# Kernel optimization log

Measured on AMD Instinct MI355X. Metric: run time of the kernel, lower is better.

The kernel has to match this reference:

```python
import jax, jax.numpy as jnp
import numpy as np

B, T, C = 2, 192, 512
H, D = 8, 64  # num_heads, head_dim; inner_dim = H*D = C


def setup_inputs() -> dict:
    key = jax.random.key(0)
    k1, k2, k3 = jax.random.split(key, 3)
    x = jax.random.normal(k1, (B, T, C), dtype=jnp.float32)
    W_in = jax.random.normal(k2, (C, 5 * H * D), dtype=jnp.float32) * 0.02
    b_in = jnp.zeros((5 * H * D,), dtype=jnp.float32)
    W_out = jax.random.normal(k3, (H * D, C), dtype=jnp.float32) * 0.02
    b_out = jnp.zeros((C,), dtype=jnp.float32)
    return {"x": x, "W_in": W_in, "b_in": b_in, "W_out": W_out, "b_out": b_out}


def _split_heads(t):
    # (B,T,H*D) -> (B,H,T,D)
    return t.reshape(B, T, H, D).transpose(0, 2, 1, 3)


def reference(x, W_in, b_in, W_out, b_out):
    scale = D ** -0.5
    proj = x @ W_in + b_in  # (B,T,5*H*D)
    q, k1, v1, k2, v2 = jnp.split(proj, 5, axis=-1)
    q = _split_heads(q) * scale
    k1 = _split_heads(k1)
    v1 = _split_heads(v1)
    k2 = _split_heads(k2)
    v2 = _split_heads(v2)
    # trilinear logits: <q_i, k1_j, k2_k> / sqrt(D), computed in fp32
    logits = jnp.einsum('bhid,bhjd,bhkd->bhijk', q, k1, k2,
                        preferred_element_type=jnp.float32)
    # softmax over the joint (j,k) axes
    attn = jax.nn.softmax(logits.reshape(B, H, T, T * T), axis=-1)
    attn = attn.reshape(B, H, T, T, T).astype(x.dtype)
    # out_i[d] = sum_{j,k} attn[i,j,k] * v1_j[d] * v2_k[d]
    out = jnp.einsum('bhijk,bhjd,bhkd->bhid', attn, v1, v2)
    y = out.transpose(0, 2, 1, 3).reshape(B, T, H * D)  # merge heads
    return y @ W_out + b_out
```

## Files before the change

kernel.cpp:

```cpp
#include <hip/hip_runtime.h>


typedef float  v4f __attribute__((ext_vector_type(4)));
typedef short  v8s __attribute__((ext_vector_type(8)));

__device__ __forceinline__ unsigned short f2bf(float f) {
  unsigned u = __float_as_uint(f);
  u += 0x7fffu + ((u >> 16) & 1u);
  return (unsigned short)(u >> 16);
}
__device__ __forceinline__ float bf2f(unsigned short b) {
  return __uint_as_float(((unsigned)b) << 16);
}

#if __has_builtin(__builtin_amdgcn_exp2f)
#define EXP2F(x) __builtin_amdgcn_exp2f(x)
#else
#define EXP2F(x) exp2f(x)
#endif

#define MFMA32(a, b, c) __builtin_amdgcn_mfma_f32_16x16x32_bf16((a), (b), (c), 0, 0, 0)

#define QSCALE 0.18033688011112042f


#define XH_OFF   589824
#define XL_OFF   786432
#define WTH_OFF  983040
#define WTL_OFF  2293760
#define WOTH_OFF 3604480
#define WOTL_OFF 3866624
#define OH_OFF   4128768
#define OL_OFF   4325376

__global__ __launch_bounds__(256) void prep_kernel(
    const float* __restrict__ x, const float* __restrict__ Win,
    const float* __restrict__ Wout, unsigned short* __restrict__ wsh) {
  const int bi = blockIdx.x, t = threadIdx.x;
  if (bi < 768) {
    const float* W; unsigned short *Th, *Tl; int R, n0, k0;
    if (bi < 640) {
      W = Win; Th = wsh + WTH_OFF; Tl = wsh + WTL_OFF; R = 2560;
      n0 = (bi % 40) << 6; k0 = (bi / 40) << 5;
    } else {
      const int idx = bi - 640;
      W = Wout; Th = wsh + WOTH_OFF; Tl = wsh + WOTL_OFF; R = 512;
      n0 = (idx & 7) << 6; k0 = (idx >> 3) << 5;
    }
    const int n = n0 + (t & 63);
    const int kg = k0 + (t >> 6) * 8;
    float v[8];
#pragma unroll
    for (int j = 0; j < 8; ++j) v[j] = W[(kg + j) * R + n];
    union { uint4 u; unsigned short us[8]; } ph, pl;
#pragma unroll
    for (int j = 0; j < 8; ++j) {
      const unsigned short h = f2bf(v[j]);
      ph.us[j] = h;
      pl.us[j] = f2bf(v[j] - bf2f(h));
    }
    *(uint4*)(Th + n * 512 + kg) = ph.u;
    *(uint4*)(Tl + n * 512 + kg) = pl.u;
  } else {
    const int flat = ((bi - 768) * 256 + t) * 8;
    const v4f v0 = *(const v4f*)(x + flat);
    const v4f v1 = *(const v4f*)(x + flat + 4);
    union { uint4 u; unsigned short us[8]; } ph, pl;
#pragma unroll
    for (int j = 0; j < 4; ++j) {
      unsigned short h = f2bf(v0[j]);
      ph.us[j] = h; pl.us[j] = f2bf(v0[j] - bf2f(h));
      h = f2bf(v1[j]);
      ph.us[4 + j] = h; pl.us[4 + j] = f2bf(v1[j] - bf2f(h));
    }
    *(uint4*)(wsh + XH_OFF + flat) = ph.u;
    *(uint4*)(wsh + XL_OFF + flat) = pl.u;
  }
}

__global__ __launch_bounds__(64) void proj_kernel(
    const unsigned short* __restrict__ wsh, const float* __restrict__ bin,
    float* __restrict__ wsf, unsigned short* __restrict__ wshd) {
  const int lane = threadIdx.x;
  const int c = lane & 15, q = lane >> 4;
  const int bm = blockIdx.x % 12, bn = blockIdx.x / 12;

  const unsigned short* ah0 = wsh + XH_OFF + (bm * 32 + c) * 512 + (q << 3);
  const unsigned short* ah1 = ah0 + 16 * 512;
  const unsigned short* al0 = wsh + XL_OFF + (bm * 32 + c) * 512 + (q << 3);
  const unsigned short* al1 = al0 + 16 * 512;
  const unsigned short* bh0 = wsh + WTH_OFF + (bn * 32 + c) * 512 + (q << 3);
  const unsigned short* bh1 = bh0 + 16 * 512;
  const unsigned short* bl0 = wsh + WTL_OFF + (bn * 32 + c) * 512 + (q << 3);
  const unsigned short* bl1 = bl0 + 16 * 512;

  const v4f z = {0.f, 0.f, 0.f, 0.f};
  v4f a00 = z, a01 = z, a10 = z, a11 = z;

  v8s cAh0 = *(const v8s*)ah0, cAh1 = *(const v8s*)ah1;
  v8s cAl0 = *(const v8s*)al0, cAl1 = *(const v8s*)al1;
  v8s cBh0 = *(const v8s*)bh0, cBh1 = *(const v8s*)bh1;
  v8s cBl0 = *(const v8s*)bl0, cBl1 = *(const v8s*)bl1;

#pragma unroll 1
  for (int ks = 0; ks < 16; ++ks) {
    v8s nAh0, nAh1, nAl0, nAl1, nBh0, nBh1, nBl0, nBl1;
    if (ks < 15) {
      const int o = (ks + 1) * 32;
      nAh0 = *(const v8s*)(ah0 + o); nAh1 = *(const v8s*)(ah1 + o);
      nAl0 = *(const v8s*)(al0 + o); nAl1 = *(const v8s*)(al1 + o);
      nBh0 = *(const v8s*)(bh0 + o); nBh1 = *(const v8s*)(bh1 + o);
      nBl0 = *(const v8s*)(bl0 + o); nBl1 = *(const v8s*)(bl1 + o);
    }
    a00 = MFMA32(cAl0, cBh0, a00); a00 = MFMA32(cAh0, cBl0, a00); a00 = MFMA32(cAh0, cBh0, a00);
    a01 = MFMA32(cAl0, cBh1, a01); a01 = MFMA32(cAh0, cBl1, a01); a01 = MFMA32(cAh0, cBh1, a01);
    a10 = MFMA32(cAl1, cBh0, a10); a10 = MFMA32(cAh1, cBl0, a10); a10 = MFMA32(cAh1, cBh0, a10);
    a11 = MFMA32(cAl1, cBh1, a11); a11 = MFMA32(cAh1, cBl1, a11); a11 = MFMA32(cAh1, cBh1, a11);
    cAh0 = nAh0; cAh1 = nAh1; cAl0 = nAl0; cAl1 = nAl1;
    cBh0 = nBh0; cBh1 = nBh1; cBl0 = nBl0; cBl1 = nBl1;
  }

  v4f accs[2][2] = {{a00, a01}, {a10, a11}};
#pragma unroll
  for (int mt = 0; mt < 2; ++mt) {
#pragma unroll
    for (int nt = 0; nt < 2; ++nt) {
      const int n = bn * 32 + nt * 16 + c;
      const int which = n >> 9, cc = n & 511, h = cc >> 6, d = cc & 63;
      const float bv = bin[n];
#pragma unroll
      for (int r = 0; r < 4; ++r) {
        const int m = bm * 32 + mt * 16 + (q << 2) + r;
        const int b = (m >= 192) ? 1 : 0;
        const int tt = m - (b ? 192 : 0);
        const int bh = b * 8 + h;
        const float val = accs[mt][nt][r] + bv;
        const int rm = ((bh * 192 + tt) << 6) + d;
        if (which == 0)      wsf[rm] = val * QSCALE;
        else if (which == 1) wshd[rm] = f2bf(val);
        else if (which == 2) wshd[393216 + ((bh << 6) + d) * 192 + tt] = f2bf(val);
        else if (which == 3) wshd[196608 + rm] = f2bf(val);
        else wsf[196608 + ((bh * 192 + tt) * 16 + (d & 15)) * 4 + (d >> 4)] = val;
      }
    }
  }
}

__global__ __launch_bounds__(256, 2) void attn_kernel(
    const float* __restrict__ wsf, const unsigned short* __restrict__ wsh,
    float* __restrict__ accp, float* __restrict__ Sp) {
  __shared__ unsigned short smem[64 * 200 + 4 * 16 * 40];
  unsigned short* V1s = smem;

  const int tid  = threadIdx.x;
  const int wv   = tid >> 6;
  const int lane = tid & 63;
  const int c    = lane & 15;
  const int quad = lane >> 4;

  const int bb = blockIdx.x;
  const int kb = bb & 3;
  const int it = (bb >> 2) % 12;
  const int bh = bb / 48;

  const unsigned short* k1g = wsh + bh * 192 * 64;
  const unsigned short* v1g = wsh + 393216 + bh * 64 * 192;
  const unsigned short* k2g = wsh + 196608 + bh * 192 * 64;
  const float*          v2g = wsf + 196608 + bh * 12288;

  for (int idx = tid; idx < 1536; idx += 256) {
    const int r = idx / 24, c8 = (idx % 24) * 8;
    *(uint4*)(V1s + r * 200 + c8) = *(const uint4*)(v1g + r * 192 + c8);
  }

  v8s k1f[12][2];
#pragma unroll
  for (int jt = 0; jt < 12; ++jt) {
    const unsigned short* kp = k1g + ((jt * 16 + c) << 6) + (quad << 3);
    k1f[jt][0] = *(const v8s*)(kp);
    k1f[jt][1] = *(const v8s*)(kp + 32);
  }

  const float* qg = wsf + ((bh * 192 + it * 16 + c) << 6) + (quad << 3);
  float q0[8], q1[8];
  {
    v4f qa = *(const v4f*)(qg), qb = *(const v4f*)(qg + 4);
    v4f qc = *(const v4f*)(qg + 32), qd = *(const v4f*)(qg + 36);
#pragma unroll
    for (int e = 0; e < 4; ++e) {
      q0[e] = qa[e]; q0[4 + e] = qb[e];
      q1[e] = qc[e]; q1[4 + e] = qd[e];
    }
  }
  __syncthreads();

  unsigned short* Pch = smem + 12800 + wv * 640;
  const v4f z = {0.f, 0.f, 0.f, 0.f};
  v4f acc0 = z, acc1 = z, acc2 = z, acc3 = z;
  float S0 = 0.f, S1 = 0.f, S2 = 0.f, S3 = 0.f;

  const int kstart = kb * 48 + wv * 12;
  union { uint4 u4; unsigned short us[8]; } kl, kh, nkl, nkh;
  kl.u4 = *(const uint4*)(k2g + (kstart << 6) + (quad << 3));
  kh.u4 = *(const uint4*)(k2g + (kstart << 6) + (quad << 3) + 32);
  v4f v2 = *(const v4f*)(v2g + ((kstart * 16 + c) << 2));

  for (int s = 0; s < 12; ++s) {
    v4f nv2;
    if (s < 11) {
      const int k2o = ((kstart + s + 1) << 6) + (quad << 3);
      nkl.u4 = *(const uint4*)(k2g + k2o);
      nkh.u4 = *(const uint4*)(k2g + k2o + 32);
      nv2 = *(const v4f*)(v2g + (((kstart + s + 1) * 16 + c) << 2));
    }

    union { v8s v; unsigned short us[8]; } af0, af1;
#pragma unroll
    for (int e = 0; e < 8; ++e) {
      af0.us[e] = f2bf(q0[e] * bf2f(kl.us[e]));
      af1.us[e] = f2bf(q1[e] * bf2f(kh.us[e]));
    }

    v4f o0 = z, o1 = z, o2 = z, o3 = z;
#pragma unroll
    for (int jp = 0; jp < 6; ++jp) {
#pragma unroll
      for (int jj2 = 0; jj2 < 2; ++jj2) {
        const int jt = jp * 2 + jj2;
        v4f Cf = MFMA32(af0.v, k1f[jt][0], z);
        Cf = MFMA32(af1.v, k1f[jt][1], Cf);
        unsigned short* wp2 = Pch + (quad << 2) * 40 + jj2 * 16 + c;
        const float p0 = EXP2F(Cf[0]), p1 = EXP2F(Cf[1]);
        const float p2 = EXP2F(Cf[2]), p3 = EXP2F(Cf[3]);
        S0 += p0; S1 += p1; S2 += p2; S3 += p3;
        wp2[0]   = (unsigned short)(__float_as_uint(p0) >> 16);
        wp2[40]  = (unsigned short)(__float_as_uint(p1) >> 16);
        wp2[80]  = (unsigned short)(__float_as_uint(p2) >> 16);
        wp2[120] = (unsigned short)(__float_as_uint(p3) >> 16);
      }
      const v8s ap = *(const v8s*)(Pch + c * 40 + (quad << 3));
      const int vcol = jp * 32 + (quad << 3);
      o0 = MFMA32(ap, *(const v8s*)(V1s + (c)      * 200 + vcol), o0);
      o1 = MFMA32(ap, *(const v8s*)(V1s + (c + 16) * 200 + vcol), o1);
      o2 = MFMA32(ap, *(const v8s*)(V1s + (c + 32) * 200 + vcol), o2);
      o3 = MFMA32(ap, *(const v8s*)(V1s + (c + 48) * 200 + vcol), o3);
    }
    acc0 += o0 * v2[0]; acc1 += o1 * v2[1]; acc2 += o2 * v2[2]; acc3 += o3 * v2[3];
    kl = nkl; kh = nkh; v2 = nv2;
  }

  __syncthreads();
  float* redA = (float*)smem;
  float* redS = (float*)smem + 4096;

#pragma unroll
  for (int m2 = 1; m2 < 16; m2 <<= 1) {
    S0 += __shfl_xor(S0, m2, 16);
    S1 += __shfl_xor(S1, m2, 16);
    S2 += __shfl_xor(S2, m2, 16);
    S3 += __shfl_xor(S3, m2, 16);
  }
  if (c == 0) {
    float* rs = redS + wv * 16 + (quad << 2);
    rs[0] = S0; rs[1] = S1; rs[2] = S2; rs[3] = S3;
  }
#pragma unroll
  for (int r = 0; r < 4; ++r) {
    float* rr = redA + wv * 1024 + (((quad << 2) + r) << 6) + c;
    rr[0] = acc0[r]; rr[16] = acc1[r]; rr[32] = acc2[r]; rr[48] = acc3[r];
  }
  __syncthreads();

  const int pbase = (bh * 12 + it) * 4 + kb;
  float* ap_out = accp + pbase * 1024;
  for (int idx = tid; idx < 1024; idx += 256)
    ap_out[idx] = redA[idx] + redA[1024 + idx] + redA[2048 + idx] + redA[3072 + idx];
  if (tid < 16)
    Sp[pbase * 16 + tid] = redS[tid] + redS[16 + tid] + redS[32 + tid] + redS[48 + tid];
}

__global__ __launch_bounds__(256) void norm_kernel(
    const float* __restrict__ accp, const float* __restrict__ Sp,
    unsigned short* __restrict__ wsh) {
  const int flat = blockIdx.x * 2048 + threadIdx.x * 8;
  const int m = flat >> 9, cc = flat & 511;
  const int b = (m >= 192) ? 1 : 0;
  const int tt = m - (b ? 192 : 0);
  const int h = cc >> 6, d0 = cc & 63;
  const int bh = b * 8 + h, it = tt >> 4, i = tt & 15;
  const int pb = (bh * 12 + it) * 4;
  const float* ap = accp + pb * 1024 + (i << 6) + d0;
  v4f a0 = *(const v4f*)(ap), a1 = *(const v4f*)(ap + 4);
  float Sv = Sp[pb * 16 + i];
#pragma unroll
  for (int kb = 1; kb < 4; ++kb) {
    a0 += *(const v4f*)(ap + kb * 1024);
    a1 += *(const v4f*)(ap + kb * 1024 + 4);
    Sv += Sp[(pb + kb) * 16 + i];
  }
  const float inv = 1.0f / Sv;
  union { uint4 u; unsigned short us[8]; } ph, pl;
#pragma unroll
  for (int j = 0; j < 4; ++j) {
    float v = a0[j] * inv;
    unsigned short hh = f2bf(v);
    ph.us[j] = hh; pl.us[j] = f2bf(v - bf2f(hh));
    v = a1[j] * inv;
    hh = f2bf(v);
    ph.us[4 + j] = hh; pl.us[4 + j] = f2bf(v - bf2f(hh));
  }
  *(uint4*)(wsh + OH_OFF + flat) = ph.u;
  *(uint4*)(wsh + OL_OFF + flat) = pl.u;
}

__global__ __launch_bounds__(64) void outp_kernel(
    const unsigned short* __restrict__ wsh, const float* __restrict__ bout,
    float* __restrict__ y) {
  const int lane = threadIdx.x;
  const int c = lane & 15, q = lane >> 4;
  const int bm = blockIdx.x % 12, bn = blockIdx.x / 12;

  const unsigned short* ah0 = wsh + OH_OFF + (bm * 32 + c) * 512 + (q << 3);
  const unsigned short* ah1 = ah0 + 16 * 512;
  const unsigned short* al0 = wsh + OL_OFF + (bm * 32 + c) * 512 + (q << 3);
  const unsigned short* al1 = al0 + 16 * 512;
  const unsigned short* bh0 = wsh + WOTH_OFF + (bn * 32 + c) * 512 + (q << 3);
  const unsigned short* bh1 = bh0 + 16 * 512;
  const unsigned short* bl0 = wsh + WOTL_OFF + (bn * 32 + c) * 512 + (q << 3);
  const unsigned short* bl1 = bl0 + 16 * 512;

  const v4f z = {0.f, 0.f, 0.f, 0.f};
  v4f a00 = z, a01 = z, a10 = z, a11 = z;

  v8s cAh0 = *(const v8s*)ah0, cAh1 = *(const v8s*)ah1;
  v8s cAl0 = *(const v8s*)al0, cAl1 = *(const v8s*)al1;
  v8s cBh0 = *(const v8s*)bh0, cBh1 = *(const v8s*)bh1;
  v8s cBl0 = *(const v8s*)bl0, cBl1 = *(const v8s*)bl1;

#pragma unroll 1
  for (int ks = 0; ks < 16; ++ks) {
    v8s nAh0, nAh1, nAl0, nAl1, nBh0, nBh1, nBl0, nBl1;
    if (ks < 15) {
      const int o = (ks + 1) * 32;
      nAh0 = *(const v8s*)(ah0 + o); nAh1 = *(const v8s*)(ah1 + o);
      nAl0 = *(const v8s*)(al0 + o); nAl1 = *(const v8s*)(al1 + o);
      nBh0 = *(const v8s*)(bh0 + o); nBh1 = *(const v8s*)(bh1 + o);
      nBl0 = *(const v8s*)(bl0 + o); nBl1 = *(const v8s*)(bl1 + o);
    }
    a00 = MFMA32(cAl0, cBh0, a00); a00 = MFMA32(cAh0, cBl0, a00); a00 = MFMA32(cAh0, cBh0, a00);
    a01 = MFMA32(cAl0, cBh1, a01); a01 = MFMA32(cAh0, cBl1, a01); a01 = MFMA32(cAh0, cBh1, a01);
    a10 = MFMA32(cAl1, cBh0, a10); a10 = MFMA32(cAh1, cBl0, a10); a10 = MFMA32(cAh1, cBh0, a10);
    a11 = MFMA32(cAl1, cBh1, a11); a11 = MFMA32(cAh1, cBl1, a11); a11 = MFMA32(cAh1, cBh1, a11);
    cAh0 = nAh0; cAh1 = nAh1; cAl0 = nAl0; cAl1 = nAl1;
    cBh0 = nBh0; cBh1 = nBh1; cBl0 = nBl0; cBl1 = nBl1;
  }

  v4f accs[2][2] = {{a00, a01}, {a10, a11}};
#pragma unroll
  for (int mt = 0; mt < 2; ++mt) {
#pragma unroll
    for (int nt = 0; nt < 2; ++nt) {
      const int n = bn * 32 + nt * 16 + c;
      const float bv = bout[n];
#pragma unroll
      for (int r = 0; r < 4; ++r) {
        const int m = bm * 32 + mt * 16 + (q << 2) + r;
        y[m * 512 + n] = accs[mt][nt][r] + bv;
      }
    }
  }
}

extern "C" void kernel_launch(void* const* d_in, const int* in_sizes, int n_in,
                              void* d_out, int out_size, void* d_ws, size_t ws_size,
                              hipStream_t stream) {
  const float* x    = (const float*)d_in[0];
  const float* Win  = (const float*)d_in[1];
  const float* bin  = (const float*)d_in[2];
  const float* Wout = (const float*)d_in[3];
  const float* bout = (const float*)d_in[4];

  float* wsf = (float*)d_ws;
  unsigned short* wsh = (unsigned short*)(wsf + 1191936);
  float* accp = wsf + 393216;
  float* Sp   = wsf + 1179648;

  prep_kernel<<<dim3(864), 256, 0, stream>>>(x, Win, Wout, wsh);
  proj_kernel<<<dim3(960), 64, 0, stream>>>(wsh, bin, wsf, wsh);
  attn_kernel<<<dim3(768), 256, 0, stream>>>(wsf, wsh, accp, Sp);
  norm_kernel<<<dim3(96), 256, 0, stream>>>(accp, Sp, wsh);
  outp_kernel<<<dim3(192), 64, 0, stream>>>(wsh, bout, (float*)d_out);
}
```

Baseline: 156.6 us.

## Restructure attention inner loop, stage K2 in LDS, transpose weights via shared tile

Several changes land together. The attention kernel now stages its K2 slice in shared memory and processes two k-rows per iteration with batched MFMAs and packed bf16 stores of P into a new 32-bit-word layout. The softmax denominator is computed with an MFMA against a ones vector, replacing the per-lane sums and shuffles, and V1 is written in a permuted column order to match the new P layout. The prep kernel transposes weights through a shared-memory tile so global accesses are coalesced, and both GEMM kernels prefetch two k-steps ahead. Together these aim to cut global load latency and scalar overhead, at the cost of more LDS use and register pressure.

New measurement: 145.1 us. -7.3%, faster.

```diff
diff --git a/kernel.cpp b/kernel.cpp
--- a/kernel.cpp
+++ b/kernel.cpp
@@ -1,4 +1,5 @@
 #include <hip/hip_runtime.h>
+#include <hip/hip_bf16.h>
 
 
 typedef float  v4f __attribute__((ext_vector_type(4)));
@@ -11,6 +12,12 @@
 }
 __device__ __forceinline__ float bf2f(unsigned short b) {
   return __uint_as_float(((unsigned)b) << 16);
+}
+__device__ __forceinline__ unsigned pack_bf16(float lo, float hi) {
+  __hip_bfloat162 t = __float22bfloat162_rn(float2{lo, hi});
+  union { __hip_bfloat162 b; unsigned u; } cv;
+  cv.b = t;
+  return cv.u;
 }
 
 #if __has_builtin(__builtin_amdgcn_exp2f)
@@ -33,9 +40,14 @@
 #define OH_OFF   4128768
 #define OL_OFF   4325376
 
+__device__ __forceinline__ int v1perm(int t) {
+  return (t & ~31) | (((t >> 2) & 3) << 3) | ((t & 3) << 1) | ((t >> 4) & 1);
+}
+
 __global__ __launch_bounds__(256) void prep_kernel(
     const float* __restrict__ x, const float* __restrict__ Win,
     const float* __restrict__ Wout, unsigned short* __restrict__ wsh) {
+  __shared__ float tile[32 * 65];
   const int bi = blockIdx.x, t = threadIdx.x;
   if (bi < 768) {
     const float* W; unsigned short *Th, *Tl; int R, n0, k0;
@@ -47,20 +59,22 @@
       W = Wout; Th = wsh + WOTH_OFF; Tl = wsh + WOTL_OFF; R = 512;
       n0 = (idx & 7) << 6; k0 = (idx >> 3) << 5;
     }
-    const int n = n0 + (t & 63);
-    const int kg = k0 + (t >> 6) * 8;
-    float v[8];
-#pragma unroll
-    for (int j = 0; j < 8; ++j) v[j] = W[(kg + j) * R + n];
+    const int n = t & 63, kq = (t >> 6) * 8;
+#pragma unroll
+    for (int j = 0; j < 8; ++j)
+      tile[(kq + j) * 65 + n] = W[(k0 + kq + j) * R + n0 + n];
+    __syncthreads();
+    const int n2 = t >> 2, ks = (t & 3) * 8;
     union { uint4 u; unsigned short us[8]; } ph, pl;
 #pragma unroll
     for (int j = 0; j < 8; ++j) {
-      const unsigned short h = f2bf(v[j]);
+      const float v = tile[(ks + j) * 65 + n2];
+      const unsigned short h = f2bf(v);
       ph.us[j] = h;
-      pl.us[j] = f2bf(v[j] - bf2f(h));
-    }
-    *(uint4*)(Th + n * 512 + kg) = ph.u;
-    *(uint4*)(Tl + n * 512 + kg) = pl.u;
+      pl.us[j] = f2bf(v - bf2f(h));
+    }
+    *(uint4*)(Th + (n0 + n2) * 512 + k0 + ks) = ph.u;
+    *(uint4*)(Tl + (n0 + n2) * 512 + k0 + ks) = pl.u;
   } else {
     const int flat = ((bi - 768) * 256 + t) * 8;
     const v4f v0 = *(const v4f*)(x + flat);
@@ -85,39 +99,39 @@
   const int c = lane & 15, q = lane >> 4;
   const int bm = blockIdx.x % 12, bn = blockIdx.x / 12;
 
-  const unsigned short* ah0 = wsh + XH_OFF + (bm * 32 + c) * 512 + (q << 3);
-  const unsigned short* ah1 = ah0 + 16 * 512;
-  const unsigned short* al0 = wsh + XL_OFF + (bm * 32 + c) * 512 + (q << 3);
-  const unsigned short* al1 = al0 + 16 * 512;
-  const unsigned short* bh0 = wsh + WTH_OFF + (bn * 32 + c) * 512 + (q << 3);
-  const unsigned short* bh1 = bh0 + 16 * 512;
-  const unsigned short* bl0 = wsh + WTL_OFF + (bn * 32 + c) * 512 + (q << 3);
-  const unsigned short* bl1 = bl0 + 16 * 512;
+  const unsigned short* base[8];
+  base[0] = wsh + XH_OFF + (bm * 32 + c) * 512 + (q << 3);
+  base[1] = base[0] + 16 * 512;
+  base[2] = wsh + XL_OFF + (bm * 32 + c) * 512 + (q << 3);
+  base[3] = base[2] + 16 * 512;
+  base[4] = wsh + WTH_OFF + (bn * 32 + c) * 512 + (q << 3);
+  base[5] = base[4] + 16 * 512;
+  base[6] = wsh + WTL_OFF + (bn * 32 + c) * 512 + (q << 3);
+  base[7] = base[6] + 16 * 512;
 
   const v4f z = {0.f, 0.f, 0.f, 0.f};
   v4f a00 = z, a01 = z, a10 = z, a11 = z;
 
-  v8s cAh0 = *(const v8s*)ah0, cAh1 = *(const v8s*)ah1;
-  v8s cAl0 = *(const v8s*)al0, cAl1 = *(const v8s*)al1;
-  v8s cBh0 = *(const v8s*)bh0, cBh1 = *(const v8s*)bh1;
-  v8s cBl0 = *(const v8s*)bl0, cBl1 = *(const v8s*)bl1;
+  v8s cur[8], nxt[8];
+#pragma unroll
+  for (int i = 0; i < 8; ++i) cur[i] = *(const v8s*)(base[i]);
+#pragma unroll
+  for (int i = 0; i < 8; ++i) nxt[i] = *(const v8s*)(base[i] + 32);
 
 #pragma unroll 1
   for (int ks = 0; ks < 16; ++ks) {
-    v8s nAh0, nAh1, nAl0, nAl1, nBh0, nBh1, nBl0, nBl1;
-    if (ks < 15) {
-      const int o = (ks + 1) * 32;
-      nAh0 = *(const v8s*)(ah0 + o); nAh1 = *(const v8s*)(ah1 + o);
-      nAl0 = *(const v8s*)(al0 + o); nAl1 = *(const v8s*)(al1 + o);
-      nBh0 = *(const v8s*)(bh0 + o); nBh1 = *(const v8s*)(bh1 + o);
-      nBl0 = *(const v8s*)(bl0 + o); nBl1 = *(const v8s*)(bl1 + o);
-    }
-    a00 = MFMA32(cAl0, cBh0, a00); a00 = MFMA32(cAh0, cBl0, a00); a00 = MFMA32(cAh0, cBh0, a00);
-    a01 = MFMA32(cAl0, cBh1, a01); a01 = MFMA32(cAh0, cBl1, a01); a01 = MFMA32(cAh0, cBh1, a01);
-    a10 = MFMA32(cAl1, cBh0, a10); a10 = MFMA32(cAh1, cBl0, a10); a10 = MFMA32(cAh1, cBh0, a10);
-    a11 = MFMA32(cAl1, cBh1, a11); a11 = MFMA32(cAh1, cBl1, a11); a11 = MFMA32(cAh1, cBh1, a11);
-    cAh0 = nAh0; cAh1 = nAh1; cAl0 = nAl0; cAl1 = nAl1;
-    cBh0 = nBh0; cBh1 = nBh1; cBl0 = nBl0; cBl1 = nBl1;
+    v8s nx2[8];
+    if (ks < 14) {
+      const int o = (ks + 2) * 32;
+#pragma unroll
+      for (int i = 0; i < 8; ++i) nx2[i] = *(const v8s*)(base[i] + o);
+    }
+    a00 = MFMA32(cur[2], cur[4], a00); a00 = MFMA32(cur[0], cur[6], a00); a00 = MFMA32(cur[0], cur[4], a00);
+    a01 = MFMA32(cur[2], cur[5], a01); a01 = MFMA32(cur[0], cur[7], a01); a01 = MFMA32(cur[0], cur[5], a01);
+    a10 = MFMA32(cur[3], cur[4], a10); a10 = MFMA32(cur[1], cur[6], a10); a10 = MFMA32(cur[1], cur[4], a10);
+    a11 = MFMA32(cur[3], cur[5], a11); a11 = MFMA32(cur[1], cur[7], a11); a11 = MFMA32(cur[1], cur[5], a11);
+#pragma unroll
+    for (int i = 0; i < 8; ++i) { cur[i] = nxt[i]; nxt[i] = nx2[i]; }
   }
 
   v4f accs[2][2] = {{a00, a01}, {a10, a11}};
@@ -138,7 +152,7 @@
         const int rm = ((bh * 192 + tt) << 6) + d;
         if (which == 0)      wsf[rm] = val * QSCALE;
         else if (which == 1) wshd[rm] = f2bf(val);
-        else if (which == 2) wshd[393216 + ((bh << 6) + d) * 192 + tt] = f2bf(val);
+        else if (which == 2) wshd[393216 + ((bh << 6) + d) * 192 + v1perm(tt)] = f2bf(val);
         else if (which == 3) wshd[196608 + rm] = f2bf(val);
         else wsf[196608 + ((bh * 192 + tt) * 16 + (d & 15)) * 4 + (d >> 4)] = val;
       }
@@ -149,8 +163,9 @@
 __global__ __launch_bounds__(256, 2) void attn_kernel(
     const float* __restrict__ wsf, const unsigned short* __restrict__ wsh,
     float* __restrict__ accp, float* __restrict__ Sp) {
-  __shared__ unsigned short smem[64 * 200 + 4 * 16 * 40];
-  unsigned short* V1s = smem;
+  __shared__ char smem[58368];
+  unsigned short* V1s = (unsigned short*)smem;
+  unsigned short* K2s = (unsigned short*)(smem + 25600);
 
   const int tid  = threadIdx.x;
   const int wv   = tid >> 6;
@@ -168,9 +183,15 @@
   const unsigned short* k2g = wsh + 196608 + bh * 192 * 64;
   const float*          v2g = wsf + 196608 + bh * 12288;
 
-  for (int idx = tid; idx < 1536; idx += 256) {
-    const int r = idx / 24, c8 = (idx % 24) * 8;
-    *(uint4*)(V1s + r * 200 + c8) = *(const uint4*)(v1g + r * 192 + c8);
+  for (int idx = tid; idx < 1920; idx += 256) {
+    if (idx < 1536) {
+      const int r = idx / 24, c8 = (idx % 24) * 8;
+      *(uint4*)(V1s + r * 200 + c8) = *(const uint4*)(v1g + r * 192 + c8);
+    } else {
+      const int j = idx - 1536;
+      const int r = j >> 3, c8 = (j & 7) * 8;
+      *(uint4*)(K2s + r * 64 + c8) = *(const uint4*)(k2g + (kb * 48 + r) * 64 + c8);
+    }
   }
 
   v8s k1f[12][2];
@@ -194,80 +215,93 @@
   }
   __syncthreads();
 
-  unsigned short* Pch = smem + 12800 + wv * 640;
+  unsigned* Pw = (unsigned*)(smem + 31744) + wv * 1664;
   const v4f z = {0.f, 0.f, 0.f, 0.f};
-  v4f acc0 = z, acc1 = z, acc2 = z, acc3 = z;
-  float S0 = 0.f, S1 = 0.f, S2 = 0.f, S3 = 0.f;
-
-  const int kstart = kb * 48 + wv * 12;
-  union { uint4 u4; unsigned short us[8]; } kl, kh, nkl, nkh;
-  kl.u4 = *(const uint4*)(k2g + (kstart << 6) + (quad << 3));
-  kh.u4 = *(const uint4*)(k2g + (kstart << 6) + (quad << 3) + 32);
-  v4f v2 = *(const v4f*)(v2g + ((kstart * 16 + c) << 2));
-
-  for (int s = 0; s < 12; ++s) {
-    v4f nv2;
-    if (s < 11) {
-      const int k2o = ((kstart + s + 1) << 6) + (quad << 3);
-      nkl.u4 = *(const uint4*)(k2g + k2o);
-      nkh.u4 = *(const uint4*)(k2g + k2o + 32);
-      nv2 = *(const v4f*)(v2g + (((kstart + s + 1) * 16 + c) << 2));
-    }
-
-    union { v8s v; unsigned short us[8]; } af0, af1;
-#pragma unroll
-    for (int e = 0; e < 8; ++e) {
-      af0.us[e] = f2bf(q0[e] * bf2f(kl.us[e]));
-      af1.us[e] = f2bf(q1[e] * bf2f(kh.us[e]));
-    }
-
-    v4f o0 = z, o1 = z, o2 = z, o3 = z;
-#pragma unroll
-    for (int jp = 0; jp < 6; ++jp) {
-#pragma unroll
-      for (int jj2 = 0; jj2 < 2; ++jj2) {
-        const int jt = jp * 2 + jj2;
-        v4f Cf = MFMA32(af0.v, k1f[jt][0], z);
-        Cf = MFMA32(af1.v, k1f[jt][1], Cf);
-        unsigned short* wp2 = Pch + (quad << 2) * 40 + jj2 * 16 + c;
-        const float p0 = EXP2F(Cf[0]), p1 = EXP2F(Cf[1]);
-        const float p2 = EXP2F(Cf[2]), p3 = EXP2F(Cf[3]);
-        S0 += p0; S1 += p1; S2 += p2; S3 += p3;
-        wp2[0]   = (unsigned short)(__float_as_uint(p0) >> 16);
-        wp2[40]  = (unsigned short)(__float_as_uint(p1) >> 16);
-        wp2[80]  = (unsigned short)(__float_as_uint(p2) >> 16);
-        wp2[120] = (unsigned short)(__float_as_uint(p3) >> 16);
+  v4f acc[4] = {z, z, z, z};
+  v4f oSA = z, oSB = z;
+  const short one = (short)0x3F80;
+  const v8s ones = {one, one, one, one, one, one, one, one};
+
+  const int kloc0 = wv * 12;
+  union U4 { uint4 u4; unsigned short us[8]; };
+  union AF { v8s v; unsigned u[4]; };
+
+#pragma unroll 1
+  for (int p = 0; p < 6; ++p) {
+    const int rA = kloc0 + 2 * p, rB = rA + 1;
+    U4 klA, khA, klB, khB;
+    klA.u4 = *(const uint4*)(K2s + rA * 64 + (quad << 3));
+    khA.u4 = *(const uint4*)(K2s + rA * 64 + (quad << 3) + 32);
+    klB.u4 = *(const uint4*)(K2s + rB * 64 + (quad << 3));
+    khB.u4 = *(const uint4*)(K2s + rB * 64 + (quad << 3) + 32);
+    const v4f v2A = *(const v4f*)(v2g + (((kb * 48 + rA) << 4) + c) * 4);
+    const v4f v2B = *(const v4f*)(v2g + (((kb * 48 + rB) << 4) + c) * 4);
+
+    AF af[2][2];
+#pragma unroll
+    for (int e = 0; e < 4; ++e) {
+      af[0][0].u[e] = pack_bf16(q0[2*e] * bf2f(klA.us[2*e]), q0[2*e+1] * bf2f(klA.us[2*e+1]));
+      af[0][1].u[e] = pack_bf16(q1[2*e] * bf2f(khA.us[2*e]), q1[2*e+1] * bf2f(khA.us[2*e+1]));
+      af[1][0].u[e] = pack_bf16(q0[2*e] * bf2f(klB.us[2*e]), q0[2*e+1] * bf2f(klB.us[2*e+1]));
+      af[1][1].u[e] = pack_bf16(q1[2*e] * bf2f(khB.us[2*e]), q1[2*e+1] * bf2f(khB.us[2*e+1]));
+    }
+
+    v4f oA[4] = {z, z, z, z}, oB[4] = {z, z, z, z};
+
+#pragma unroll
+    for (int h = 0; h < 2; ++h) {
+#pragma unroll
+      for (int kk = 0; kk < 2; ++kk) {
+        v4f C[6];
+#pragma unroll
+        for (int jj = 0; jj < 6; ++jj) {
+          const int jt = h * 6 + jj;
+          v4f t0 = MFMA32(af[kk][0].v, k1f[jt][0], z);
+          C[jj] = MFMA32(af[kk][1].v, k1f[jt][1], t0);
+        }
+#pragma unroll
+        for (int jj = 0; jj < 6; ++jj)
+#pragma unroll
+          for (int r = 0; r < 4; ++r) C[jj][r] = EXP2F(C[jj][r]);
+#pragma unroll
+        for (int m = 0; m < 3; ++m)
+#pragma unroll
+          for (int r = 0; r < 4; ++r)
+            Pw[kk * 832 + ((quad << 2) + r) * 52 + m * 16 + c] =
+                pack_bf16(C[2*m][r], C[2*m+1][r]);
       }
-      const v8s ap = *(const v8s*)(Pch + c * 40 + (quad << 3));
-      const int vcol = jp * 32 + (quad << 3);
-      o0 = MFMA32(ap, *(const v8s*)(V1s + (c)      * 200 + vcol), o0);
-      o1 = MFMA32(ap, *(const v8s*)(V1s + (c + 16) * 200 + vcol), o1);
-      o2 = MFMA32(ap, *(const v8s*)(V1s + (c + 32) * 200 + vcol), o2);
-      o3 = MFMA32(ap, *(const v8s*)(V1s + (c + 48) * 200 + vcol), o3);
-    }
-    acc0 += o0 * v2[0]; acc1 += o1 * v2[1]; acc2 += o2 * v2[2]; acc3 += o3 * v2[3];
-    kl = nkl; kh = nkh; v2 = nv2;
+#pragma unroll
+      for (int m = 0; m < 3; ++m) {
+        const v8s apA = *(const v8s*)(Pw + c * 52 + m * 16 + (quad << 2));
+        const v8s apB = *(const v8s*)(Pw + 832 + c * 52 + m * 16 + (quad << 2));
+        oSA = MFMA32(apA, ones, oSA);
+        oSB = MFMA32(apB, ones, oSB);
+        const int vcol = (h * 3 + m) * 32 + (quad << 3);
+#pragma unroll
+        for (int t = 0; t < 4; ++t) {
+          const v8s vf = *(const v8s*)(V1s + (c + 16 * t) * 200 + vcol);
+          oA[t] = MFMA32(apA, vf, oA[t]);
+          oB[t] = MFMA32(apB, vf, oB[t]);
+        }
+      }
+    }
+#pragma unroll
+    for (int t = 0; t < 4; ++t) acc[t] += oA[t] * v2A[t] + oB[t] * v2B[t];
   }
 
   __syncthreads();
   float* redA = (float*)smem;
   float* redS = (float*)smem + 4096;
 
-#pragma unroll
-  for (int m2 = 1; m2 < 16; m2 <<= 1) {
-    S0 += __shfl_xor(S0, m2, 16);
-    S1 += __shfl_xor(S1, m2, 16);
-    S2 += __shfl_xor(S2, m2, 16);
-    S3 += __shfl_xor(S3, m2, 16);
-  }
   if (c == 0) {
     float* rs = redS + wv * 16 + (quad << 2);
-    rs[0] = S0; rs[1] = S1; rs[2] = S2; rs[3] = S3;
+#pragma unroll
+    for (int r = 0; r < 4; ++r) rs[r] = oSA[r] + oSB[r];
   }
 #pragma unroll
   for (int r = 0; r < 4; ++r) {
     float* rr = redA + wv * 1024 + (((quad << 2) + r) << 6) + c;
-    rr[0] = acc0[r]; rr[16] = acc1[r]; rr[32] = acc2[r]; rr[48] = acc3[r];
+    rr[0] = acc[0][r]; rr[16] = acc[1][r]; rr[32] = acc[2][r]; rr[48] = acc[3][r];
   }
   __syncthreads();
 
@@ -320,39 +354,39 @@
   const int c = lane & 15, q = lane >> 4;
   const int bm = blockIdx.x % 12, bn = blockIdx.x / 12;
 
-  const unsigned short* ah0 = wsh + OH_OFF + (bm * 32 + c) * 512 + (q << 3);
-  const unsigned short* ah1 = ah0 + 16 * 512;
-  const unsigned short* al0 = wsh + OL_OFF + (bm * 32 + c) * 512 + (q << 3);
-  const unsigned short* al1 = al0 + 16 * 512;
-  const unsigned short* bh0 = wsh + WOTH_OFF + (bn * 32 + c) * 512 + (q << 3);
-  const unsigned short* bh1 = bh0 + 16 * 512;
-  const unsigned short* bl0 = wsh + WOTL_OFF + (bn * 32 + c) * 512 + (q << 3);
-  const unsigned short* bl1 = bl0 + 16 * 512;
+  const unsigned short* base[8];
+  base[0] = wsh + OH_OFF + (bm * 32 + c) * 512 + (q << 3);
+  base[1] = base[0] + 16 * 512;
+  base[2] = wsh + OL_OFF + (bm * 32 + c) * 512 + (q << 3);
+  base[3] = base[2] + 16 * 512;
+  base[4] = wsh + WOTH_OFF + (bn * 32 + c) * 512 + (q << 3);
+  base[5] = base[4] + 16 * 512;
+  base[6] = wsh + WOTL_OFF + (bn * 32 + c) * 512 + (q << 3);
+  base[7] = base[6] + 16 * 512;
 
   const v4f z = {0.f, 0.f, 0.f, 0.f};
   v4f a00 = z, a01 = z, a10 = z, a11 = z;
 
-  v8s cAh0 = *(const v8s*)ah0, cAh1 = *(const v8s*)ah1;
-  v8s cAl0 = *(const v8s*)al0, cAl1 = *(const v8s*)al1;
-  v8s cBh0 = *(const v8s*)bh0, cBh1 = *(const v8s*)bh1;
-  v8s cBl0 = *(const v8s*)bl0, cBl1 = *(const v8s*)bl1;
+  v8s cur[8], nxt[8];
+#pragma unroll
+  for (int i = 0; i < 8; ++i) cur[i] = *(const v8s*)(base[i]);
+#pragma unroll
+  for (int i = 0; i < 8; ++i) nxt[i] = *(const v8s*)(base[i] + 32);
 
 #pragma unroll 1
   for (int ks = 0; ks < 16; ++ks) {
-    v8s nAh0, nAh1, nAl0, nAl1, nBh0, nBh1, nBl0, nBl1;
-    if (ks < 15) {
-      const int o = (ks + 1) * 32;
-      nAh0 = *(const v8s*)(ah0 + o); nAh1 = *(const v8s*)(ah1 + o);
-      nAl0 = *(const v8s*)(al0 + o); nAl1 = *(const v8s*)(al1 + o);
-      nBh0 = *(const v8s*)(bh0 + o); nBh1 = *(const v8s*)(bh1 + o);
-      nBl0 = *(const v8s*)(bl0 + o); nBl1 = *(const v8s*)(bl1 + o);
-    }
-    a00 = MFMA32(cAl0, cBh0, a00); a00 = MFMA32(cAh0, cBl0, a00); a00 = MFMA32(cAh0, cBh0, a00);
-    a01 = MFMA32(cAl0, cBh1, a01); a01 = MFMA32(cAh0, cBl1, a01); a01 = MFMA32(cAh0, cBh1, a01);
-    a10 = MFMA32(cAl1, cBh0, a10); a10 = MFMA32(cAh1, cBl0, a10); a10 = MFMA32(cAh1, cBh0, a10);
-    a11 = MFMA32(cAl1, cBh1, a11); a11 = MFMA32(cAh1, cBl1, a11); a11 = MFMA32(cAh1, cBh1, a11);
-    cAh0 = nAh0; cAh1 = nAh1; cAl0 = nAl0; cAl1 = nAl1;
-    cBh0 = nBh0; cBh1 = nBh1; cBl0 = nBl0; cBl1 = nBl1;
+    v8s nx2[8];
+    if (ks < 14) {
+      const int o = (ks + 2) * 32;
+#pragma unroll
+      for (int i = 0; i < 8; ++i) nx2[i] = *(const v8s*)(base[i] + o);
+    }
+    a00 = MFMA32(cur[2], cur[4], a00); a00 = MFMA32(cur[0], cur[6], a00); a00 = MFMA32(cur[0], cur[4], a00);
+    a01 = MFMA32(cur[2], cur[5], a01); a01 = MFMA32(cur[0], cur[7], a01); a01 = MFMA32(cur[0], cur[5], a01);
+    a10 = MFMA32(cur[3], cur[4], a10); a10 = MFMA32(cur[1], cur[6], a10); a10 = MFMA32(cur[1], cur[4], a10);
+    a11 = MFMA32(cur[3], cur[5], a11); a11 = MFMA32(cur[1], cur[7], a11); a11 = MFMA32(cur[1], cur[5], a11);
+#pragma unroll
+    for (int i = 0; i < 8; ++i) { cur[i] = nxt[i]; nxt[i] = nx2[i]; }
   }
 
   v4f accs[2][2] = {{a00, a01}, {a10, a11}};
```
